# Kernel tuning notes

Measured on AMD Instinct MI355X. Metric: run time of the kernel, lower is better.

## Reference

```python
import jax, jax.numpy as jnp
import numpy as np

N_NODES = 100000
N_EDGES = 1600000
D_IN = 128
D_H = [128, 128]


def setup_inputs() -> dict:
    key = jax.random.key(0)
    ks = jax.random.split(key, 7)
    x = jax.random.normal(ks[0], (N_NODES, D_IN), dtype=jnp.float32)
    edge_index = jax.random.randint(ks[1], (2, N_EDGES), 0, N_NODES, dtype=jnp.int64)
    # Glorot-style init for GCNConv weights, zero bias (PyG defaults)
    s1 = (6.0 / (D_IN + D_H[0])) ** 0.5
    s2 = (6.0 / (D_H[0] + D_H[1])) ** 0.5
    W1 = jax.random.uniform(ks[2], (D_IN, D_H[0]), jnp.float32, -s1, s1)
    b1 = jnp.zeros((D_H[0],), jnp.float32)
    W2 = jax.random.uniform(ks[3], (D_H[0], D_H[1]), jnp.float32, -s2, s2)
    b2 = jnp.zeros((D_H[1],), jnp.float32)
    return {"x": x, "edge_index": edge_index, "W1": W1, "b1": b1, "W2": W2, "b2": b2}


def _gcn_conv(x, src, dst, W, b, n_nodes):
    """PyG GCNConv: add self-loops, symmetric normalization, scatter-add aggregate."""
    h = x @ W  # [N, D_out]
    # degree at destination including the implicit self-loop
    deg = jax.ops.segment_sum(jnp.ones(src.shape[0], h.dtype), dst, num_segments=n_nodes) + 1.0
    dinv = jax.lax.rsqrt(deg)  # deg >= 1 always (self-loop)
    coef = dinv[src] * dinv[dst]  # [E]
    msg = h[src] * coef[:, None]  # gather + scale, [E, D_out]
    agg = jax.ops.segment_sum(msg, dst, num_segments=n_nodes)
    # self-loop contribution: dinv[i]^2 * h[i]
    agg = agg + h * (dinv * dinv)[:, None]
    return agg + b


def reference(x, edge_index, W1, b1, W2, b2):
    # eval-mode forward: dropout layers are identity (training=False)
    src, dst = edge_index[0], edge_index[1]
    n = x.shape[0]
    h = jax.nn.relu(_gcn_conv(x, src, dst, W1, b1, n))
    h = jax.nn.relu(_gcn_conv(h, src, dst, W2, b2, n))
    return h
```

## Files before the change

### kernel.cpp

```cpp
#include <hip/hip_runtime.h>


#define NN 100000
#define NE 1600000
#define DD 128
#define SCAN_NB 391

__device__ __forceinline__ unsigned f2bf(float f) {
  unsigned u = __float_as_uint(f);
  return (u + 0x7fffu + ((u >> 16) & 1u)) >> 16;
}
__device__ __forceinline__ unsigned pack2(float lo, float hi) {
  return f2bf(lo) | (f2bf(hi) << 16);
}


__global__ __launch_bounds__(256) void zero_i32(int* __restrict__ p, int n) {
  int i = blockIdx.x * 256 + threadIdx.x;
  if (i < n) p[i] = 0;
}

__global__ __launch_bounds__(256) void deg_rank(const int* __restrict__ edst,
                                                int* __restrict__ cnt,
                                                int* __restrict__ rank) {
  int e = blockIdx.x * 256 + threadIdx.x;
  if (e < NE) rank[e] = atomicAdd(&cnt[edst[e]], 1);
}

__global__ __launch_bounds__(256) void scan_block_sums(const int* __restrict__ cnt,
                                                       int* __restrict__ bsum) {
  __shared__ int s[256];
  int t = threadIdx.x;
  int i = blockIdx.x * 256 + t;
  s[t] = (i < NN) ? cnt[i] : 0;
  __syncthreads();
  for (int off = 128; off > 0; off >>= 1) {
    if (t < off) s[t] += s[t + off];
    __syncthreads();
  }
  if (t == 0) bsum[blockIdx.x] = s[0];
}

__global__ __launch_bounds__(512) void scan_partials(int* __restrict__ bsum) {
  __shared__ int s[512];
  int t = threadIdx.x;
  int v = (t < SCAN_NB) ? bsum[t] : 0;
  s[t] = v;
  __syncthreads();
  for (int off = 1; off < 512; off <<= 1) {
    int a = (t >= off) ? s[t - off] : 0;
    __syncthreads();
    s[t] += a;
    __syncthreads();
  }
  if (t < SCAN_NB) bsum[t] = s[t] - v;
}

__global__ __launch_bounds__(256) void scan_write(const int* __restrict__ cnt,
                                                  const int* __restrict__ bsum,
                                                  int* __restrict__ rowptr,
                                                  float* __restrict__ dinv) {
  __shared__ int s[256];
  int t = threadIdx.x;
  int i = blockIdx.x * 256 + t;
  int v = (i < NN) ? cnt[i] : 0;
  s[t] = v;
  __syncthreads();
  for (int off = 1; off < 256; off <<= 1) {
    int a = (t >= off) ? s[t - off] : 0;
    __syncthreads();
    s[t] += a;
    __syncthreads();
  }
  int excl = s[t] - v + bsum[blockIdx.x];
  if (i < NN) {
    rowptr[i] = excl;
    dinv[i] = rsqrtf((float)v + 1.0f);
  }
  if (i == NN - 1) rowptr[NN] = excl + v;
}


__global__ __launch_bounds__(256) void build_csr(const int* __restrict__ esrc,
                                                 const int* __restrict__ edst,
                                                 const int* __restrict__ rank,
                                                 const int* __restrict__ rowptr,
                                                 int* __restrict__ col) {
  int e = blockIdx.x * 256 + threadIdx.x;
  if (e < NE) col[rowptr[edst[e]] + rank[e]] = esrc[e];
}

__global__ __launch_bounds__(256) void gemm128(const float* __restrict__ X,
                                               const float* __restrict__ W,
                                               const float* __restrict__ dinv,
                                               unsigned short* __restrict__ G) {
  __shared__ float ws2[32][128];
  __shared__ float xs[64][36];
  const int t = threadIdx.x;
  const int tx = t & 15;
  const int ty = t >> 4;
  const int row0 = blockIdx.x * 64;
  float acc[4][8];
#pragma unroll
  for (int i = 0; i < 4; ++i)
#pragma unroll
    for (int j = 0; j < 8; ++j) acc[i][j] = 0.f;

  for (int kc = 0; kc < 128; kc += 32) {
#pragma unroll
    for (int i = 0; i < 4; ++i) {
      int idx = i * 256 + t;
      int kk = idx >> 5;
      int c4 = idx & 31;
      *(float4*)&ws2[kk][c4 * 4] = *(const float4*)&W[(kc + kk) * 128 + c4 * 4];
    }
#pragma unroll
    for (int i = 0; i < 2; ++i) {
      int idx = i * 256 + t;
      int r = idx >> 3;
      int c4 = idx & 7;
      int grow = row0 + r;
      if (grow > NN - 1) grow = NN - 1;
      *(float4*)&xs[r][c4 * 4] = *(const float4*)&X[grow * 128 + kc + c4 * 4];
    }
    __syncthreads();
#pragma unroll
    for (int kk = 0; kk < 32; kk += 4) {
      float4 a0 = *(float4*)&xs[ty * 4 + 0][kk];
      float4 a1 = *(float4*)&xs[ty * 4 + 1][kk];
      float4 a2 = *(float4*)&xs[ty * 4 + 2][kk];
      float4 a3 = *(float4*)&xs[ty * 4 + 3][kk];
#pragma unroll
      for (int j = 0; j < 4; ++j) {
        float4 b0 = *(float4*)&ws2[kk + j][tx * 4];
        float4 b1 = *(float4*)&ws2[kk + j][64 + tx * 4];
        float a[4] = {j == 0 ? a0.x : j == 1 ? a0.y : j == 2 ? a0.z : a0.w,
                      j == 0 ? a1.x : j == 1 ? a1.y : j == 2 ? a1.z : a1.w,
                      j == 0 ? a2.x : j == 1 ? a2.y : j == 2 ? a2.z : a2.w,
                      j == 0 ? a3.x : j == 1 ? a3.y : j == 2 ? a3.z : a3.w};
#pragma unroll
        for (int i = 0; i < 4; ++i) {
          acc[i][0] += a[i] * b0.x;
          acc[i][1] += a[i] * b0.y;
          acc[i][2] += a[i] * b0.z;
          acc[i][3] += a[i] * b0.w;
          acc[i][4] += a[i] * b1.x;
          acc[i][5] += a[i] * b1.y;
          acc[i][6] += a[i] * b1.z;
          acc[i][7] += a[i] * b1.w;
        }
      }
    }
    __syncthreads();
  }
#pragma unroll
  for (int i = 0; i < 4; ++i) {
    int row = row0 + ty * 4 + i;
    if (row < NN) {
      float di = dinv[row];
      uint2 p0 = make_uint2(pack2(acc[i][0] * di, acc[i][1] * di),
                            pack2(acc[i][2] * di, acc[i][3] * di));
      uint2 p1 = make_uint2(pack2(acc[i][4] * di, acc[i][5] * di),
                            pack2(acc[i][6] * di, acc[i][7] * di));
      *(uint2*)&G[row * 128 + tx * 4] = p0;
      *(uint2*)&G[row * 128 + 64 + tx * 4] = p1;
    }
  }
}

__global__ __launch_bounds__(256) void aggregate(const unsigned short* __restrict__ G,
                                                 const int* __restrict__ rowptr,
                                                 const int* __restrict__ col,
                                                 const float* __restrict__ dinv,
                                                 const float* __restrict__ bias,
                                                 float* __restrict__ out) {
  int gid = blockIdx.x * 256 + threadIdx.x;
  int node = gid >> 5;
  int lane = gid & 31;
  const int off = lane * 4;

  uint2 us = *(const uint2*)&G[node * DD + off];
  float4 acc;
  acc.x = __uint_as_float(us.x << 16);
  acc.y = __uint_as_float(us.x & 0xffff0000u);
  acc.z = __uint_as_float(us.y << 16);
  acc.w = __uint_as_float(us.y & 0xffff0000u);

  int e = rowptr[node];
  int e1 = rowptr[node + 1];
  for (; e + 3 < e1; e += 4) {
    int s0 = col[e + 0];
    int s1 = col[e + 1];
    int s2 = col[e + 2];
    int s3 = col[e + 3];
    uint2 u0 = *(const uint2*)&G[s0 * DD + off];
    uint2 u1 = *(const uint2*)&G[s1 * DD + off];
    uint2 u2 = *(const uint2*)&G[s2 * DD + off];
    uint2 u3 = *(const uint2*)&G[s3 * DD + off];
    acc.x += __uint_as_float(u0.x << 16);
    acc.y += __uint_as_float(u0.x & 0xffff0000u);
    acc.z += __uint_as_float(u0.y << 16);
    acc.w += __uint_as_float(u0.y & 0xffff0000u);
    acc.x += __uint_as_float(u1.x << 16);
    acc.y += __uint_as_float(u1.x & 0xffff0000u);
    acc.z += __uint_as_float(u1.y << 16);
    acc.w += __uint_as_float(u1.y & 0xffff0000u);
    acc.x += __uint_as_float(u2.x << 16);
    acc.y += __uint_as_float(u2.x & 0xffff0000u);
    acc.z += __uint_as_float(u2.y << 16);
    acc.w += __uint_as_float(u2.y & 0xffff0000u);
    acc.x += __uint_as_float(u3.x << 16);
    acc.y += __uint_as_float(u3.x & 0xffff0000u);
    acc.z += __uint_as_float(u3.y << 16);
    acc.w += __uint_as_float(u3.y & 0xffff0000u);
  }
  for (; e < e1; ++e) {
    int s0 = col[e];
    uint2 u0 = *(const uint2*)&G[s0 * DD + off];
    acc.x += __uint_as_float(u0.x << 16);
    acc.y += __uint_as_float(u0.x & 0xffff0000u);
    acc.z += __uint_as_float(u0.y << 16);
    acc.w += __uint_as_float(u0.y & 0xffff0000u);
  }

  float di = dinv[node];
  float4 bv = *(const float4*)&bias[off];
  acc.x = fmaxf(acc.x * di + bv.x, 0.f);
  acc.y = fmaxf(acc.y * di + bv.y, 0.f);
  acc.z = fmaxf(acc.z * di + bv.z, 0.f);
  acc.w = fmaxf(acc.w * di + bv.w, 0.f);
  *(float4*)&out[node * DD + off] = acc;
}


extern "C" void kernel_launch(void* const* d_in, const int* in_sizes, int n_in,
                              void* d_out, int out_size, void* d_ws, size_t ws_size,
                              hipStream_t stream) {
  const float* x  = (const float*)d_in[0];
  const int*   ei = (const int*)d_in[1];
  const float* W1 = (const float*)d_in[2];
  const float* b1 = (const float*)d_in[3];
  const float* W2 = (const float*)d_in[4];
  const float* b2 = (const float*)d_in[5];
  float* out = (float*)d_out;

  const int* esrc = ei;
  const int* edst = ei + NE;

  char* w = (char*)d_ws;
  int*   cnt    = (int*)w;    w += ((NN + 1023) & ~1023) * 4;
  float* dinv   = (float*)w;  w += ((NN + 1023) & ~1023) * 4;
  int*   rowptr = (int*)w;    w += ((NN + 1 + 1023) & ~1023) * 4;
  int*   bsum   = (int*)w;    w += 512 * 4;
  int*   rank   = (int*)w;    w += (size_t)NE * 4;
  int*   col    = (int*)w;    w += (size_t)NE * 4;
  unsigned short* G = (unsigned short*)w;

  const int nb_n = (NN + 255) / 256;
  const int nb_e = (NE + 255) / 256;

  zero_i32<<<nb_n, 256, 0, stream>>>(cnt, NN);
  deg_rank<<<nb_e, 256, 0, stream>>>(edst, cnt, rank);
  scan_block_sums<<<SCAN_NB, 256, 0, stream>>>(cnt, bsum);
  scan_partials<<<1, 512, 0, stream>>>(bsum);
  scan_write<<<SCAN_NB, 256, 0, stream>>>(cnt, bsum, rowptr, dinv);
  build_csr<<<nb_e, 256, 0, stream>>>(esrc, edst, rank, rowptr, col);

  gemm128<<<(NN + 63) / 64, 256, 0, stream>>>(x, W1, dinv, G);
  aggregate<<<NN * 32 / 256, 256, 0, stream>>>(G, rowptr, col, dinv, b1, out);

  gemm128<<<(NN + 63) / 64, 256, 0, stream>>>(out, W2, dinv, G);
  aggregate<<<NN * 32 / 256, 256, 0, stream>>>(G, rowptr, col, dinv, b2, out);
}
```

Measured before the change: 421.8 us.

## Fuse degree counting into first GEMM and split atomic counters four ways

The degree/rank atomic pass now runs inside the first GEMM kernel, with counters split across four replicas to reduce atomic contention. The dinv scaling of the first GEMM output moves into a later pass that is merged with CSR construction in one launch, and dinv is recomputed from the offset array instead of being stored. This removes separate kernel launches and overlaps the atomic traffic with GEMM work. In exchange it adds an extra read-modify-write pass over G and a 4x larger counter array, which costs more to zero and scan.

```diff
diff --git a/kernel.cpp b/kernel.cpp
--- a/kernel.cpp
+++ b/kernel.cpp
@@ -5,6 +5,9 @@
 #define NE 1600000
 #define DD 128
 #define SCAN_NB 391
+#define GEMM_NB 1563
+#define CSR_NB 6250
+#define SCALE_NB 3125
 
 __device__ __forceinline__ unsigned f2bf(float f) {
   unsigned u = __float_as_uint(f);
@@ -13,93 +16,44 @@
 __device__ __forceinline__ unsigned pack2(float lo, float hi) {
   return f2bf(lo) | (f2bf(hi) << 16);
 }
-
+__device__ __forceinline__ unsigned scale2(unsigned u, float s) {
+  float lo = __uint_as_float(u << 16) * s;
+  float hi = __uint_as_float(u & 0xffff0000u) * s;
+  return pack2(lo, hi);
+}
 
 __global__ __launch_bounds__(256) void zero_i32(int* __restrict__ p, int n) {
   int i = blockIdx.x * 256 + threadIdx.x;
   if (i < n) p[i] = 0;
 }
 
-__global__ __launch_bounds__(256) void deg_rank(const int* __restrict__ edst,
-                                                int* __restrict__ cnt,
-                                                int* __restrict__ rank) {
-  int e = blockIdx.x * 256 + threadIdx.x;
-  if (e < NE) rank[e] = atomicAdd(&cnt[edst[e]], 1);
-}
-
-__global__ __launch_bounds__(256) void scan_block_sums(const int* __restrict__ cnt,
-                                                       int* __restrict__ bsum) {
-  __shared__ int s[256];
-  int t = threadIdx.x;
-  int i = blockIdx.x * 256 + t;
-  s[t] = (i < NN) ? cnt[i] : 0;
-  __syncthreads();
-  for (int off = 128; off > 0; off >>= 1) {
-    if (t < off) s[t] += s[t + off];
-    __syncthreads();
-  }
-  if (t == 0) bsum[blockIdx.x] = s[0];
-}
-
-__global__ __launch_bounds__(512) void scan_partials(int* __restrict__ bsum) {
-  __shared__ int s[512];
-  int t = threadIdx.x;
-  int v = (t < SCAN_NB) ? bsum[t] : 0;
-  s[t] = v;
-  __syncthreads();
-  for (int off = 1; off < 512; off <<= 1) {
-    int a = (t >= off) ? s[t - off] : 0;
-    __syncthreads();
-    s[t] += a;
-    __syncthreads();
-  }
-  if (t < SCAN_NB) bsum[t] = s[t] - v;
-}
-
-__global__ __launch_bounds__(256) void scan_write(const int* __restrict__ cnt,
-                                                  const int* __restrict__ bsum,
-                                                  int* __restrict__ rowptr,
-                                                  float* __restrict__ dinv) {
-  __shared__ int s[256];
-  int t = threadIdx.x;
-  int i = blockIdx.x * 256 + t;
-  int v = (i < NN) ? cnt[i] : 0;
-  s[t] = v;
-  __syncthreads();
-  for (int off = 1; off < 256; off <<= 1) {
-    int a = (t >= off) ? s[t - off] : 0;
-    __syncthreads();
-    s[t] += a;
-    __syncthreads();
-  }
-  int excl = s[t] - v + bsum[blockIdx.x];
-  if (i < NN) {
-    rowptr[i] = excl;
-    dinv[i] = rsqrtf((float)v + 1.0f);
-  }
-  if (i == NN - 1) rowptr[NN] = excl + v;
-}
-
-
-__global__ __launch_bounds__(256) void build_csr(const int* __restrict__ esrc,
-                                                 const int* __restrict__ edst,
-                                                 const int* __restrict__ rank,
-                                                 const int* __restrict__ rowptr,
-                                                 int* __restrict__ col) {
-  int e = blockIdx.x * 256 + threadIdx.x;
-  if (e < NE) col[rowptr[edst[e]] + rank[e]] = esrc[e];
-}
-
-__global__ __launch_bounds__(256) void gemm128(const float* __restrict__ X,
-                                               const float* __restrict__ W,
-                                               const float* __restrict__ dinv,
-                                               unsigned short* __restrict__ G) {
+__global__ __launch_bounds__(256) void gemm_deg(const float* __restrict__ X,
+                                                const float* __restrict__ W,
+                                                const int* __restrict__ edst,
+                                                int* __restrict__ cntR,
+                                                int* __restrict__ rank,
+                                                unsigned short* __restrict__ G) {
+  const int t = threadIdx.x;
+  const int b = blockIdx.x;
+
+  int myrank[4];
+  const int eb = b * 1024;
+#pragma unroll
+  for (int i = 0; i < 4; ++i) {
+    int e = eb + i * 256 + t;
+    if (e < NE) {
+      int d = edst[e];
+      int r = (t + i) & 3;
+      int loc = atomicAdd(&cntR[r * NN + d], 1);
+      myrank[i] = (loc << 2) | r;
+    }
+  }
+
   __shared__ float ws2[32][128];
   __shared__ float xs[64][36];
-  const int t = threadIdx.x;
   const int tx = t & 15;
   const int ty = t >> 4;
-  const int row0 = blockIdx.x * 64;
+  const int row0 = b * 64;
   float acc[4][8];
 #pragma unroll
   for (int i = 0; i < 4; ++i)
@@ -157,21 +111,126 @@
   for (int i = 0; i < 4; ++i) {
     int row = row0 + ty * 4 + i;
     if (row < NN) {
-      float di = dinv[row];
-      uint2 p0 = make_uint2(pack2(acc[i][0] * di, acc[i][1] * di),
-                            pack2(acc[i][2] * di, acc[i][3] * di));
-      uint2 p1 = make_uint2(pack2(acc[i][4] * di, acc[i][5] * di),
-                            pack2(acc[i][6] * di, acc[i][7] * di));
+      uint2 p0 = make_uint2(pack2(acc[i][0], acc[i][1]), pack2(acc[i][2], acc[i][3]));
+      uint2 p1 = make_uint2(pack2(acc[i][4], acc[i][5]), pack2(acc[i][6], acc[i][7]));
       *(uint2*)&G[row * 128 + tx * 4] = p0;
       *(uint2*)&G[row * 128 + 64 + tx * 4] = p1;
     }
   }
-}
+
+#pragma unroll
+  for (int i = 0; i < 4; ++i) {
+    int e = eb + i * 256 + t;
+    if (e < NE) rank[e] = myrank[i];
+  }
+}
+
+
+__global__ __launch_bounds__(256) void scan_l1(const int* __restrict__ cntR,
+                                               int* __restrict__ bsum) {
+  __shared__ int s[256];
+  int t = threadIdx.x;
+  int node = blockIdx.x * 256 + t;
+  int sum = 0;
+  if (node < NN) {
+#pragma unroll
+    for (int r = 0; r < 4; ++r) sum += cntR[r * NN + node];
+  }
+  s[t] = sum;
+  __syncthreads();
+  for (int off = 128; off > 0; off >>= 1) {
+    if (t < off) s[t] += s[t + off];
+    __syncthreads();
+  }
+  if (t == 0) bsum[blockIdx.x] = s[0];
+}
+
+__global__ __launch_bounds__(512) void scan_partials(int* __restrict__ bsum) {
+  __shared__ int s[512];
+  int t = threadIdx.x;
+  int v = (t < SCAN_NB) ? bsum[t] : 0;
+  s[t] = v;
+  __syncthreads();
+  for (int off = 1; off < 512; off <<= 1) {
+    int a = (t >= off) ? s[t - off] : 0;
+    __syncthreads();
+    s[t] += a;
+    __syncthreads();
+  }
+  if (t < SCAN_NB) bsum[t] = s[t] - v;
+}
+
+__global__ __launch_bounds__(256) void scan_l2(const int* __restrict__ cntR,
+                                               const int* __restrict__ bsum,
+                                               int* __restrict__ offp) {
+  __shared__ int s[256];
+  int t = threadIdx.x;
+  int node = blockIdx.x * 256 + t;
+  int v[4] = {0, 0, 0, 0};
+  if (node < NN) {
+#pragma unroll
+    for (int r = 0; r < 4; ++r) v[r] = cntR[r * NN + node];
+  }
+  int tot = v[0] + v[1] + v[2] + v[3];
+  s[t] = tot;
+  __syncthreads();
+  for (int o = 1; o < 256; o <<= 1) {
+    int a = (t >= o) ? s[t - o] : 0;
+    __syncthreads();
+    s[t] += a;
+    __syncthreads();
+  }
+  int base = bsum[blockIdx.x] + s[t] - tot;
+  if (node < NN) {
+    int acc = base;
+#pragma unroll
+    for (int r = 0; r < 4; ++r) {
+      offp[node * 4 + r] = acc;
+      acc += v[r];
+    }
+    if (node == NN - 1) offp[NN * 4] = acc;
+  }
+}
+
+
+__global__ __launch_bounds__(256) void csr_scale(const int* __restrict__ esrc,
+                                                 const int* __restrict__ edst,
+                                                 const int* __restrict__ rank,
+                                                 const int* __restrict__ offp,
+                                                 int* __restrict__ col,
+                                                 unsigned short* __restrict__ G) {
+  int b = blockIdx.x;
+  int t = threadIdx.x;
+  if (b < CSR_NB) {
+    int e = b * 256 + t;
+    int d = edst[e];
+    int rk = rank[e];
+    int pos = offp[d * 4 + (rk & 3)] + (rk >> 2);
+    col[pos] = esrc[e];
+  } else {
+    int sb = b - CSR_NB;
+    int base = sb * 4096 + t * 16;
+    int row = base >> 7;
+    int d0 = offp[row * 4];
+    int d1 = offp[row * 4 + 4];
+    float di = rsqrtf((float)(d1 - d0) + 1.0f);
+    uint4* p = (uint4*)&G[base];
+#pragma unroll
+    for (int q = 0; q < 2; ++q) {
+      uint4 u = p[q];
+      u.x = scale2(u.x, di);
+      u.y = scale2(u.y, di);
+      u.z = scale2(u.z, di);
+      u.w = scale2(u.w, di);
+      p[q] = u;
+    }
+  }
+}
+
 
 __global__ __launch_bounds__(256) void aggregate(const unsigned short* __restrict__ G,
-                                                 const int* __restrict__ rowptr,
+                                                 const int* __restrict__ offp,
                                                  const int* __restrict__ col,
-                                                 const float* __restrict__ dinv,
                                                  const float* __restrict__ bias,
                                                  float* __restrict__ out) {
   int gid = blockIdx.x * 256 + threadIdx.x;
@@ -179,6 +238,10 @@
   int lane = gid & 31;
   const int off = lane * 4;
 
+  int e = offp[node * 4];
+  int e1 = offp[node * 4 + 4];
+  float di = rsqrtf((float)(e1 - e) + 1.0f);
+
   uint2 us = *(const uint2*)&G[node * DD + off];
   float4 acc;
   acc.x = __uint_as_float(us.x << 16);
@@ -186,8 +249,6 @@
   acc.z = __uint_as_float(us.y << 16);
   acc.w = __uint_as_float(us.y & 0xffff0000u);
 
-  int e = rowptr[node];
-  int e1 = rowptr[node + 1];
   for (; e + 3 < e1; e += 4) {
     int s0 = col[e + 0];
     int s1 = col[e + 1];
@@ -223,13 +284,93 @@
     acc.w += __uint_as_float(u0.y & 0xffff0000u);
   }
 
-  float di = dinv[node];
   float4 bv = *(const float4*)&bias[off];
   acc.x = fmaxf(acc.x * di + bv.x, 0.f);
   acc.y = fmaxf(acc.y * di + bv.y, 0.f);
   acc.z = fmaxf(acc.z * di + bv.z, 0.f);
   acc.w = fmaxf(acc.w * di + bv.w, 0.f);
   *(float4*)&out[node * DD + off] = acc;
+}
+
+
+__global__ __launch_bounds__(256) void gemm128(const float* __restrict__ X,
+                                               const float* __restrict__ W,
+                                               const int* __restrict__ offp,
+                                               unsigned short* __restrict__ G) {
+  __shared__ float ws2[32][128];
+  __shared__ float xs[64][36];
+  const int t = threadIdx.x;
+  const int tx = t & 15;
+  const int ty = t >> 4;
+  const int row0 = blockIdx.x * 64;
+  float acc[4][8];
+#pragma unroll
+  for (int i = 0; i < 4; ++i)
+#pragma unroll
+    for (int j = 0; j < 8; ++j) acc[i][j] = 0.f;
+
+  for (int kc = 0; kc < 128; kc += 32) {
+#pragma unroll
+    for (int i = 0; i < 4; ++i) {
+      int idx = i * 256 + t;
+      int kk = idx >> 5;
+      int c4 = idx & 31;
+      *(float4*)&ws2[kk][c4 * 4] = *(const float4*)&W[(kc + kk) * 128 + c4 * 4];
+    }
+#pragma unroll
+    for (int i = 0; i < 2; ++i) {
+      int idx = i * 256 + t;
+      int r = idx >> 3;
+      int c4 = idx & 7;
+      int grow = row0 + r;
+      if (grow > NN - 1) grow = NN - 1;
+      *(float4*)&xs[r][c4 * 4] = *(const float4*)&X[grow * 128 + kc + c4 * 4];
+    }
+    __syncthreads();
+#pragma unroll
+    for (int kk = 0; kk < 32; kk += 4) {
+      float4 a0 = *(float4*)&xs[ty * 4 + 0][kk];
+      float4 a1 = *(float4*)&xs[ty * 4 + 1][kk];
+      float4 a2 = *(float4*)&xs[ty * 4 + 2][kk];
+      float4 a3 = *(float4*)&xs[ty * 4 + 3][kk];
+#pragma unroll
+      for (int j = 0; j < 4; ++j) {
+        float4 b0 = *(float4*)&ws2[kk + j][tx * 4];
+        float4 b1 = *(float4*)&ws2[kk + j][64 + tx * 4];
+        float a[4] = {j == 0 ? a0.x : j == 1 ? a0.y : j == 2 ? a0.z : a0.w,
+                      j == 0 ? a1.x : j == 1 ? a1.y : j == 2 ? a1.z : a1.w,
+                      j == 0 ? a2.x : j == 1 ? a2.y : j == 2 ? a2.z : a2.w,
+                      j == 0 ? a3.x : j == 1 ? a3.y : j == 2 ? a3.z : a3.w};
+#pragma unroll
+        for (int i = 0; i < 4; ++i) {
+          acc[i][0] += a[i] * b0.x;
+          acc[i][1] += a[i] * b0.y;
+          acc[i][2] += a[i] * b0.z;
+          acc[i][3] += a[i] * b0.w;
+          acc[i][4] += a[i] * b1.x;
+          acc[i][5] += a[i] * b1.y;
+          acc[i][6] += a[i] * b1.z;
+          acc[i][7] += a[i] * b1.w;
+        }
+      }
+    }
+    __syncthreads();
+  }
+#pragma unroll
+  for (int i = 0; i < 4; ++i) {
+    int row = row0 + ty * 4 + i;
+    if (row < NN) {
+      int d0 = offp[row * 4];
+      int d1 = offp[row * 4 + 4];
+      float di = rsqrtf((float)(d1 - d0) + 1.0f);
+      uint2 p0 = make_uint2(pack2(acc[i][0] * di, acc[i][1] * di),
+                            pack2(acc[i][2] * di, acc[i][3] * di));
+      uint2 p1 = make_uint2(pack2(acc[i][4] * di, acc[i][5] * di),
+                            pack2(acc[i][6] * di, acc[i][7] * di));
+      *(uint2*)&G[row * 128 + tx * 4] = p0;
+      *(uint2*)&G[row * 128 + 64 + tx * 4] = p1;
+    }
+  }
 }
 
 
@@ -248,27 +389,25 @@
   const int* edst = ei + NE;
 
   char* w = (char*)d_ws;
-  int*   cnt    = (int*)w;    w += ((NN + 1023) & ~1023) * 4;
-  float* dinv   = (float*)w;  w += ((NN + 1023) & ~1023) * 4;
-  int*   rowptr = (int*)w;    w += ((NN + 1 + 1023) & ~1023) * 4;
-  int*   bsum   = (int*)w;    w += 512 * 4;
-  int*   rank   = (int*)w;    w += (size_t)NE * 4;
-  int*   col    = (int*)w;    w += (size_t)NE * 4;
+  int* cntR = (int*)w;  w += (size_t)(NN * 4) * 4;
+  int* offp = (int*)w;  w += (size_t)(NN * 4 + 16) * 4;
+  int* bsum = (int*)w;  w += 512 * 4;
+  int* rank = (int*)w;  w += (size_t)NE * 4;
+  int* col  = (int*)w;  w += (size_t)NE * 4;
   unsigned short* G = (unsigned short*)w;
 
-  const int nb_n = (NN + 255) / 256;
-  const int nb_e = (NE + 255) / 256;
-
-  zero_i32<<<nb_n, 256, 0, stream>>>(cnt, NN);
-  deg_rank<<<nb_e, 256, 0, stream>>>(edst, cnt, rank);
-  scan_block_sums<<<SCAN_NB, 256, 0, stream>>>(cnt, bsum);
+  zero_i32<<<GEMM_NB, 256, 0, stream>>>(cntR, NN * 4);
+
+  gemm_deg<<<GEMM_NB, 256, 0, stream>>>(x, W1, edst, cntR, rank, G);
+
+  scan_l1<<<SCAN_NB, 256, 0, stream>>>(cntR, bsum);
   scan_partials<<<1, 512, 0, stream>>>(bsum);
-  scan_write<<<SCAN_NB, 256, 0, stream>>>(cnt, bsum, rowptr, dinv);
-  build_csr<<<nb_e, 256, 0, stream>>>(esrc, edst, rank, rowptr, col);
-
-  gemm128<<<(NN + 63) / 64, 256, 0, stream>>>(x, W1, dinv, G);
-  aggregate<<<NN * 32 / 256, 256, 0, stream>>>(G, rowptr, col, dinv, b1, out);
-
-  gemm128<<<(NN + 63) / 64, 256, 0, stream>>>(out, W2, dinv, G);
-  aggregate<<<NN * 32 / 256, 256, 0, stream>>>(G, rowptr, col, dinv, b2, out);
-}
+  scan_l2<<<SCAN_NB, 256, 0, stream>>>(cntR, bsum, offp);
+
+  csr_scale<<<CSR_NB + SCALE_NB, 256, 0, stream>>>(esrc, edst, rank, offp, col, G);
+
+  aggregate<<<NN * 32 / 256, 256, 0, stream>>>(G, offp, col, b1, out);
+
+  gemm128<<<GEMM_NB, 256, 0, stream>>>(out, W2, offp, G);
+  aggregate<<<NN * 32 / 256, 256, 0, stream>>>(G, offp, col, b2, out);
+}
```

Measured after the change: 461.9 us. 1.09x slower.

## Split degree counters into four sub-buckets to reduce atomic contention

Applied to the files above, without the earlier changes.

Degree counting now spreads each destination's atomic increments across four separate counter arrays, chosen by thread and edge index, so fewer atomics collide on one address. Ranks encode the sub-bucket, and the scan writes a per-node, per-bucket offset table that the CSR build uses to place each edge. The aggregate kernel computes dinv from the row length instead of loading it. This adds memory traffic for the four-way counters and offsets, and the 4x-strided offp reads in aggregate are less compact than the old rowptr reads.

```diff
diff --git a/kernel.cpp b/kernel.cpp
--- a/kernel.cpp
+++ b/kernel.cpp
@@ -5,6 +5,9 @@
 #define NE 1600000
 #define DD 128
 #define SCAN_NB 391
+#define DEG_NB 1563
+#define GEMM_NB 1563
+#define CSR_NB 6250
 
 __device__ __forceinline__ unsigned f2bf(float f) {
   unsigned u = __float_as_uint(f);
@@ -14,25 +17,39 @@
   return f2bf(lo) | (f2bf(hi) << 16);
 }
 
-
 __global__ __launch_bounds__(256) void zero_i32(int* __restrict__ p, int n) {
   int i = blockIdx.x * 256 + threadIdx.x;
   if (i < n) p[i] = 0;
 }
 
 __global__ __launch_bounds__(256) void deg_rank(const int* __restrict__ edst,
-                                                int* __restrict__ cnt,
+                                                int* __restrict__ cntR,
                                                 int* __restrict__ rank) {
-  int e = blockIdx.x * 256 + threadIdx.x;
-  if (e < NE) rank[e] = atomicAdd(&cnt[edst[e]], 1);
-}
-
-__global__ __launch_bounds__(256) void scan_block_sums(const int* __restrict__ cnt,
-                                                       int* __restrict__ bsum) {
+  int base = blockIdx.x * 1024 + threadIdx.x;
+#pragma unroll
+  for (int i = 0; i < 4; ++i) {
+    int e = base + i * 256;
+    if (e < NE) {
+      int d = edst[e];
+      int r = (threadIdx.x + i) & 3;
+      int loc = atomicAdd(&cntR[r * NN + d], 1);
+      rank[e] = (loc << 2) | r;
+    }
+  }
+}
+
+
+__global__ __launch_bounds__(256) void scan_l1(const int* __restrict__ cntR,
+                                               int* __restrict__ bsum) {
   __shared__ int s[256];
   int t = threadIdx.x;
-  int i = blockIdx.x * 256 + t;
-  s[t] = (i < NN) ? cnt[i] : 0;
+  int node = blockIdx.x * 256 + t;
+  int sum = 0;
+  if (node < NN) {
+#pragma unroll
+    for (int r = 0; r < 4; ++r) sum += cntR[r * NN + node];
+  }
+  s[t] = sum;
   __syncthreads();
   for (int off = 128; off > 0; off >>= 1) {
     if (t < off) s[t] += s[t + off];
@@ -56,38 +73,50 @@
   if (t < SCAN_NB) bsum[t] = s[t] - v;
 }
 
-__global__ __launch_bounds__(256) void scan_write(const int* __restrict__ cnt,
-                                                  const int* __restrict__ bsum,
-                                                  int* __restrict__ rowptr,
-                                                  float* __restrict__ dinv) {
+__global__ __launch_bounds__(256) void scan_l2(const int* __restrict__ cntR,
+                                               const int* __restrict__ bsum,
+                                               int* __restrict__ offp,
+                                               float* __restrict__ dinv) {
   __shared__ int s[256];
   int t = threadIdx.x;
-  int i = blockIdx.x * 256 + t;
-  int v = (i < NN) ? cnt[i] : 0;
-  s[t] = v;
+  int node = blockIdx.x * 256 + t;
+  int v[4] = {0, 0, 0, 0};
+  if (node < NN) {
+#pragma unroll
+    for (int r = 0; r < 4; ++r) v[r] = cntR[r * NN + node];
+  }
+  int tot = v[0] + v[1] + v[2] + v[3];
+  s[t] = tot;
   __syncthreads();
-  for (int off = 1; off < 256; off <<= 1) {
-    int a = (t >= off) ? s[t - off] : 0;
+  for (int o = 1; o < 256; o <<= 1) {
+    int a = (t >= o) ? s[t - o] : 0;
     __syncthreads();
     s[t] += a;
     __syncthreads();
   }
-  int excl = s[t] - v + bsum[blockIdx.x];
-  if (i < NN) {
-    rowptr[i] = excl;
-    dinv[i] = rsqrtf((float)v + 1.0f);
-  }
-  if (i == NN - 1) rowptr[NN] = excl + v;
+  int base = bsum[blockIdx.x] + s[t] - tot;
+  if (node < NN) {
+    int acc = base;
+#pragma unroll
+    for (int r = 0; r < 4; ++r) {
+      offp[node * 4 + r] = acc;
+      acc += v[r];
+    }
+    dinv[node] = rsqrtf((float)tot + 1.0f);
+    if (node == NN - 1) offp[NN * 4] = acc;
+  }
 }
 
 
 __global__ __launch_bounds__(256) void build_csr(const int* __restrict__ esrc,
                                                  const int* __restrict__ edst,
                                                  const int* __restrict__ rank,
-                                                 const int* __restrict__ rowptr,
+                                                 const int* __restrict__ offp,
                                                  int* __restrict__ col) {
   int e = blockIdx.x * 256 + threadIdx.x;
-  if (e < NE) col[rowptr[edst[e]] + rank[e]] = esrc[e];
+  int d = edst[e];
+  int rk = rank[e];
+  col[offp[d * 4 + (rk & 3)] + (rk >> 2)] = esrc[e];
 }
 
 __global__ __launch_bounds__(256) void gemm128(const float* __restrict__ X,
@@ -168,10 +197,10 @@
   }
 }
 
+
 __global__ __launch_bounds__(256) void aggregate(const unsigned short* __restrict__ G,
-                                                 const int* __restrict__ rowptr,
+                                                 const int* __restrict__ offp,
                                                  const int* __restrict__ col,
-                                                 const float* __restrict__ dinv,
                                                  const float* __restrict__ bias,
                                                  float* __restrict__ out) {
   int gid = blockIdx.x * 256 + threadIdx.x;
@@ -179,6 +208,10 @@
   int lane = gid & 31;
   const int off = lane * 4;
 
+  int e = offp[node * 4];
+  int e1 = offp[node * 4 + 4];
+  float di = rsqrtf((float)(e1 - e) + 1.0f);
+
   uint2 us = *(const uint2*)&G[node * DD + off];
   float4 acc;
   acc.x = __uint_as_float(us.x << 16);
@@ -186,8 +219,6 @@
   acc.z = __uint_as_float(us.y << 16);
   acc.w = __uint_as_float(us.y & 0xffff0000u);
 
-  int e = rowptr[node];
-  int e1 = rowptr[node + 1];
   for (; e + 3 < e1; e += 4) {
     int s0 = col[e + 0];
     int s1 = col[e + 1];
@@ -223,7 +254,6 @@
     acc.w += __uint_as_float(u0.y & 0xffff0000u);
   }
 
-  float di = dinv[node];
   float4 bv = *(const float4*)&bias[off];
   acc.x = fmaxf(acc.x * di + bv.x, 0.f);
   acc.y = fmaxf(acc.y * di + bv.y, 0.f);
@@ -248,27 +278,24 @@
   const int* edst = ei + NE;
 
   char* w = (char*)d_ws;
-  int*   cnt    = (int*)w;    w += ((NN + 1023) & ~1023) * 4;
-  float* dinv   = (float*)w;  w += ((NN + 1023) & ~1023) * 4;
-  int*   rowptr = (int*)w;    w += ((NN + 1 + 1023) & ~1023) * 4;
-  int*   bsum   = (int*)w;    w += 512 * 4;
-  int*   rank   = (int*)w;    w += (size_t)NE * 4;
-  int*   col    = (int*)w;    w += (size_t)NE * 4;
+  int*   cntR = (int*)w;  w += (size_t)(NN * 4) * 4;
+  int*   offp = (int*)w;  w += (size_t)(NN * 4 + 16) * 4;
+  int*   bsum = (int*)w;  w += 512 * 4;
+  float* dinv = (float*)w; w += ((NN + 1023) & ~1023) * 4;
+  int*   rank = (int*)w;  w += (size_t)NE * 4;
+  int*   col  = (int*)w;  w += (size_t)NE * 4;
   unsigned short* G = (unsigned short*)w;
 
-  const int nb_n = (NN + 255) / 256;
-  const int nb_e = (NE + 255) / 256;
-
-  zero_i32<<<nb_n, 256, 0, stream>>>(cnt, NN);
-  deg_rank<<<nb_e, 256, 0, stream>>>(edst, cnt, rank);
-  scan_block_sums<<<SCAN_NB, 256, 0, stream>>>(cnt, bsum);
+  zero_i32<<<GEMM_NB, 256, 0, stream>>>(cntR, NN * 4);
+  deg_rank<<<DEG_NB, 256, 0, stream>>>(edst, cntR, rank);
+  scan_l1<<<SCAN_NB, 256, 0, stream>>>(cntR, bsum);
   scan_partials<<<1, 512, 0, stream>>>(bsum);
-  scan_write<<<SCAN_NB, 256, 0, stream>>>(cnt, bsum, rowptr, dinv);
-  build_csr<<<nb_e, 256, 0, stream>>>(esrc, edst, rank, rowptr, col);
-
-  gemm128<<<(NN + 63) / 64, 256, 0, stream>>>(x, W1, dinv, G);
-  aggregate<<<NN * 32 / 256, 256, 0, stream>>>(G, rowptr, col, dinv, b1, out);
-
-  gemm128<<<(NN + 63) / 64, 256, 0, stream>>>(out, W2, dinv, G);
-  aggregate<<<NN * 32 / 256, 256, 0, stream>>>(G, rowptr, col, dinv, b2, out);
-}
+  scan_l2<<<SCAN_NB, 256, 0, stream>>>(cntR, bsum, offp, dinv);
+  build_csr<<<CSR_NB, 256, 0, stream>>>(esrc, edst, rank, offp, col);
+
+  gemm128<<<GEMM_NB, 256, 0, stream>>>(x, W1, dinv, G);
+  aggregate<<<NN * 32 / 256, 256, 0, stream>>>(G, offp, col, b1, out);
+
+  gemm128<<<GEMM_NB, 256, 0, stream>>>(out, W2, dinv, G);
+  aggregate<<<NN * 32 / 256, 256, 0, stream>>>(G, offp, col, b2, out);
+}
```

Result: slower. 463.4 us (+9.9%).
